# Kernel optimization log

Hardware: AMD Instinct MI355X
Metric: run time of the kernel (lower is better)

Reference implementation:

```python
import jax, jax.numpy as jnp
import numpy as np

EMA_DECAY = 0.99
LOSS_SCALE = 10.0
COMMIT_COEF = 0.25
EPS = 1e-5


def setup_inputs() -> dict:
    key = jax.random.key(0)
    k1, k2, k3 = jax.random.split(key, 3)
    B, S, D, K = 8, 2048, 256, 4096
    z = jax.random.normal(k1, (B, S, D), dtype=jnp.float32)
    attention_mask = jnp.ones((B, S), dtype=jnp.float32)
    codebook = jax.random.normal(k2, (K, D), dtype=jnp.float32)
    ema_count = jnp.ones((K,), dtype=jnp.float32)
    ema_weight = codebook.copy()  # torch: ema_weight = codebook.weight.data.clone()
    return {"z": z, "attention_mask": attention_mask, "codebook": codebook,
            "ema_count": ema_count, "ema_weight": ema_weight}


def reference(z, attention_mask, codebook, ema_count, ema_weight):
    B, S, D = z.shape
    K = codebook.shape[0]
    flat = z.reshape(-1, D)                       # [N, D], N = B*S
    # squared euclidean distances to codebook: [N, K]
    distances = (jnp.sum(flat * flat, axis=1, keepdims=True)
                 - 2.0 * flat @ codebook.T
                 + jnp.sum(codebook * codebook, axis=1))
    indices = jnp.argmin(distances, axis=1)       # [N] int
    quantized = codebook[indices].reshape(B, S, D)

    # EMA accumulation (training path). Instead of materializing the NxK
    # one-hot and doing encodings.T @ flat, use segment sums (same math).
    mask_flat = attention_mask.reshape(-1)        # [N]
    n = jax.ops.segment_sum(mask_flat, indices, num_segments=K)            # [K]
    dw = jax.ops.segment_sum(flat * mask_flat[:, None], indices,
                             num_segments=K)                               # [K, D]

    new_count = ema_count * EMA_DECAY + (1.0 - EMA_DECAY) * n
    total = jnp.sum(new_count)
    new_count = (new_count + EPS) / (total + K * EPS) * total
    new_weight = ema_weight * EMA_DECAY + (1.0 - EMA_DECAY) * dw

    # commitment loss (quantized detached)
    loss_tok = jnp.mean((z - jax.lax.stop_gradient(quantized)) ** 2, axis=-1)  # [B,S]
    quantize_loss = LOSS_SCALE * COMMIT_COEF * jnp.sum(loss_tok * attention_mask) / jnp.sum(attention_mask)

    # straight-through estimator
    out = z + jax.lax.stop_gradient(quantized - z)
    return out, indices, quantize_loss, new_count, new_weight
```

## Files before the change

kernel.cpp:

```cpp
#include <hip/hip_runtime.h>
#include <hip/hip_fp16.h>
#include <cstdint>
#include <cstddef>


#define N_TOK 16384
#define DIM   256
#define K_CB  4096

typedef _Float16 h8    __attribute__((ext_vector_type(8)));
typedef float    f32x4 __attribute__((ext_vector_type(4)));
typedef float    f32x16 __attribute__((ext_vector_type(16)));

#define WS_ZF      0u
#define WS_CP      8388608u
#define WS_CN      10485760u
#define WS_NRM     10502144u
#define WS_CAND    10633216u
#define WS_COUNT   12730368u
#define WS_SLOTS   12746752u
#define WS_NACC    29523968u
#define WS_NB      29540352u
#define WS_LPART   29540368u
#define WS_MPART   29556752u
#define WS_NBPART  29573136u

__device__ __forceinline__ void gload_lds16(const void* g, void* l) {
  __builtin_amdgcn_global_load_lds(
      (const __attribute__((address_space(1))) uint32_t*)g,
      (__attribute__((address_space(3))) uint32_t*)l, 16, 0, 0);
}

__global__ void vq_split_z(const float* __restrict__ z, unsigned short* __restrict__ zf,
                           float2* __restrict__ nrm) {
  int t = blockIdx.x * 256 + threadIdx.x;
  int tok = t >> 5, c = t & 31;
  const float4* zp = reinterpret_cast<const float4*>(z) + (size_t)tok * 64 + c * 2;
  float4 va = zp[0], vb = zp[1];
  float x[8] = {va.x, va.y, va.z, va.w, vb.x, vb.y, vb.z, vb.w};
  union { _Float16 h[8]; uint4 u; } a;
  float s1 = 0.f, s2 = 0.f;
#pragma unroll
  for (int i = 0; i < 8; ++i) {
    _Float16 h1 = (_Float16)x[i];
    float lo = (x[i] - (float)h1) * 2048.0f;
    a.h[i] = h1;
    s1 += (float)h1 * (float)h1;
    s2 += lo * lo;
  }
  size_t off = (size_t)(tok >> 7) * 65536u + (size_t)(c >> 1) * 4096u
             + (size_t)(tok & 127) * 32u + (size_t)(c & 1) * 16u;
  *reinterpret_cast<uint4*>((unsigned char*)zf + off) = a.u;
#pragma unroll
  for (int o = 1; o < 32; o <<= 1) { s1 += __shfl_xor(s1, o); s2 += __shfl_xor(s2, o); }
  if (c == 0) nrm[tok] = make_float2(sqrtf(s1), sqrtf(s2));
}

__global__ void vq_split_c(const float* __restrict__ cb, unsigned short* __restrict__ cp1,
                           float* __restrict__ cn1, float2* __restrict__ nbpart) {
  __shared__ float sm1[4], sm2[4];
  int w = threadIdx.x >> 6, l = threadIdx.x & 63;
  int row = blockIdx.x * 4 + w;
  float4 v = reinterpret_cast<const float4*>(cb)[row * 64 + l];
  float x[4] = {v.x, v.y, v.z, v.w};
  union { _Float16 h[4]; ushort4 u; } a;
  double ss = 0.0;
  float s1 = 0.f, s2 = 0.f;
#pragma unroll
  for (int i = 0; i < 4; ++i) {
    _Float16 h1 = (_Float16)x[i];
    float lo = (x[i] - (float)h1) * 2048.0f;
    a.h[i] = h1;
    s1 += (float)h1 * (float)h1;
    s2 += lo * lo;
    ss += (double)x[i] * (double)x[i];
  }
  reinterpret_cast<ushort4*>(cp1)[row * 64 + l] = a.u;
  for (int off = 1; off < 64; off <<= 1) {
    s1 += __shfl_xor(s1, off); s2 += __shfl_xor(s2, off); ss += __shfl_xor(ss, off);
  }
  if (l == 0) {
    cn1[row] = (float)ss;
    sm1[w] = s1; sm2[w] = s2;
  }
  __syncthreads();
  if (threadIdx.x == 0) {
    float m1 = fmaxf(fmaxf(sm1[0], sm1[1]), fmaxf(sm1[2], sm1[3]));
    float m2 = fmaxf(fmaxf(sm2[0], sm2[1]), fmaxf(sm2[2], sm2[3]));
    nbpart[blockIdx.x] = make_float2(sqrtf(m1), sqrtf(m2));
  }
}

__global__ void vq_nb_reduce(const float2* __restrict__ nbpart, float* __restrict__ nb) {
  __shared__ float r1[256], r2[256];
  int tid = threadIdx.x;
  float m1 = 0.f, m2 = 0.f;
  for (int i = tid; i < 1024; i += 256) {
    float2 p = nbpart[i];
    m1 = fmaxf(m1, p.x); m2 = fmaxf(m2, p.y);
  }
  r1[tid] = m1; r2[tid] = m2; __syncthreads();
  for (int s = 128; s > 0; s >>= 1) {
    if (tid < s) { r1[tid] = fmaxf(r1[tid], r1[tid + s]); r2[tid] = fmaxf(r2[tid], r2[tid + s]); }
    __syncthreads();
  }
  if (tid == 0) { nb[0] = r1[0]; nb[1] = r2[0]; }
}

__global__ __launch_bounds__(256, 2) void vq_scan(
    const unsigned short* __restrict__ zf, const unsigned short* __restrict__ cp,
    const float* __restrict__ cn1, const float2* __restrict__ nrm,
    float2* __restrict__ cand) {
  __shared__ __align__(1024) unsigned char cbl[2][16384];
  __shared__ __align__(16) float cnl[2][32];

  const int bid  = blockIdx.x;
  const int wgid = (bid & 7) * 256 + (bid >> 3);
  const int tg   = wgid >> 4;
  const int es   = wgid & 15;
  const int tok0 = tg * 128;
  const int e0b  = es * 256;

  const int tx = threadIdx.x;
  const int w = tx >> 6, l = tx & 63;
  const int r = l & 31, h = l >> 5;

  const unsigned char* zg = (const unsigned char*)zf + (size_t)tg * 65536u
                            + (unsigned)(w * 1024 + r * 32 + h * 16);
  h8 zfr[16];
#pragma unroll
  for (int kt = 0; kt < 16; ++kt) {
    const void* p = zg + kt * 4096;
    asm volatile("global_load_dwordx4 %0, %1, off"
                 : "=v"(zfr[kt]) : "v"(p));
  }
  float znr = nrm[tok0 + w * 32 + r].x;
  const float zn = znr * znr;

  const unsigned char* cpb = (const unsigned char*)cp;
  unsigned lo = 0xFFFFFFFFu, hi = 0xFFFFFFFFu;

#define STAGE(T1)                                                           \
  {                                                                         \
    const int e0n = e0b + (T1) * 32;                                        \
    _Pragma("unroll")                                                       \
    for (int j = 0; j < 4; ++j) {                                           \
      int row = (w * 4 + j) * 2 + h;                                        \
      int lc  = r ^ row;                                                    \
      gload_lds16(cpb + (size_t)(e0n + row) * 512 + lc * 16,                \
                  &cbl[(T1) & 1][(w * 4 + j) * 1024]);                      \
    }                                                                       \
    if (tx < 8)                                                             \
      gload_lds16((const unsigned char*)cn1 + (size_t)e0n * 4 + tx * 16,    \
                  &cnl[(T1) & 1][0]);                                       \
  }

#define INIT_ACC(C, BUF)                                                    \
  {                                                                         \
    _Pragma("unroll")                                                       \
    for (int g = 0; g < 4; ++g) {                                           \
      f32x4 cnv = *reinterpret_cast<const f32x4*>(&cnl[(BUF)][g * 8 + 4 * h]); \
      _Pragma("unroll")                                                     \
      for (int q = 0; q < 4; ++q) (C)[g * 4 + q] = -0.5f * (zn + cnv[q]);   \
    }                                                                       \
  }

#define MFMA_TILE(C, BUF)                                                   \
  {                                                                         \
    _Pragma("unroll")                                                       \
    for (int kt = 0; kt < 16; ++kt) {                                       \
      int sc = (kt * 2 + h) ^ r;                                            \
      h8 af = *reinterpret_cast<const h8*>(&cbl[(BUF)][r * 512 + sc * 16]); \
      (C) = __builtin_amdgcn_mfma_f32_32x32x16_f16(af, zfr[kt], (C), 0, 0, 0); \
    }                                                                       \
  }

#define SELECT_PREV(P, TPREV)                                               \
  {                                                                         \
    _Pragma("unroll")                                                       \
    for (int i = 0; i < 16; ++i) {                                          \
      unsigned eloc = (unsigned)((TPREV) * 32 + ((i & 3) + 8 * (i >> 2) + 4 * h)); \
      unsigned key = (__float_as_uint((P)[i]) & 0xFFFFFF00u) | eloc;        \
      unsigned mx = lo > key ? lo : key;                                    \
      lo = lo < key ? lo : key;                                             \
      hi = hi < mx ? hi : mx;                                               \
    }                                                                       \
  }

#define TILE_BODY(T, CUR, PRV, DOSEL)                                       \
  {                                                                         \
    if ((T) < 7) STAGE((T) + 1);                                            \
    INIT_ACC(CUR, (T) & 1);                                                 \
    MFMA_TILE(CUR, (T) & 1);                                                \
    if (DOSEL) SELECT_PREV(PRV, (T) - 1);                                   \
    __syncthreads();                                                        \
  }

  STAGE(0);
  __syncthreads();

  f32x16 accA, accB;
  for (int tt = 0; tt < 4; ++tt) {
    TILE_BODY(2 * tt,     accA, accB, (tt > 0));
    TILE_BODY(2 * tt + 1, accB, accA, true);
  }
  SELECT_PREV(accB, 7);

#undef TILE_BODY
#undef SELECT_PREV
#undef MFMA_TILE
#undef INIT_ACC
#undef STAGE

  {
    unsigned olo = __shfl_xor(lo, 32), ohi = __shfl_xor(hi, 32);
    unsigned mx = lo > olo ? lo : olo;
    lo = lo < olo ? lo : olo;
    hi = hi < ohi ? hi : ohi;
    hi = hi < mx ? hi : mx;
    if (h == 0) {
      int token = tok0 + w * 32 + r;
      cand[(size_t)token * 16 + es] =
          make_float2(__uint_as_float(lo), __uint_as_float(hi));
    }
  }
}

__global__ void vq_merge(
    const float2* __restrict__ cand, const float* __restrict__ z,
    const float* __restrict__ mask, const float* __restrict__ codebook,
    const float2* __restrict__ nrm, const float* __restrict__ nb,
    float* __restrict__ out0, float* __restrict__ out_idx,
    int* __restrict__ count, int* __restrict__ slots,
    float* __restrict__ loss_part, float* __restrict__ mask_part) {
  __shared__ float ls[4], ms[4];
  int w = threadIdx.x >> 6, l = threadIdx.x & 63;
  int token = blockIdx.x * 4 + w;

  float2 rec = cand[(size_t)token * 16 + (l & 15)];
  unsigned k1 = __float_as_uint(rec.x), k2 = __float_as_uint(rec.y);
  float rv1 = -2.0f * __uint_as_float(k1 & 0xFFFFFF00u);
  float rv2 = -2.0f * __uint_as_float(k2 & 0xFFFFFF00u);
  int   ri1 = (l & 15) * 256 + (int)(k1 & 0xFFu);
  int   ri2 = (l & 15) * 256 + (int)(k2 & 0xFFu);
  float m_a = rv1;
  for (int o = 1; o < 16; o <<= 1) m_a = fminf(m_a, __shfl_xor(m_a, o));

  float2 nh = nrm[token];
  float NB1 = nb[0], NB2 = nb[1];
  float E = 2.0f * ((nh.x * NB2 + nh.y * NB1) * (1.0f / 2048.0f)
                    + nh.y * NB2 * (1.0f / 4194304.0f));
  float thr = m_a * 1.0001f + 2.0f * E * 1.05f + 0.1f;

  float4 zv = reinterpret_cast<const float4*>(z)[(size_t)token * 64 + l];

  unsigned long long c1 = __ballot((l < 16) && (rv1 <= thr));
  unsigned long long c2 = __ballot((l < 16) && (rv2 <= thr));
  double bd = 1e300; int bi = 0x7fffffff;
  while (c1 | c2) {
    int k;
    if (c1) { int s = __ffsll(c1) - 1; c1 &= c1 - 1; k = __shfl(ri1, s); }
    else    { int s = __ffsll(c2) - 1; c2 &= c2 - 1; k = __shfl(ri2, s); }
    float4 cv = reinterpret_cast<const float4*>(codebook)[(size_t)k * 64 + l];
    double d0 = (double)zv.x - cv.x, d1 = (double)zv.y - cv.y;
    double d2 = (double)zv.z - cv.z, d3 = (double)zv.w - cv.w;
    double dd = d0 * d0 + d1 * d1 + d2 * d2 + d3 * d3;
    for (int o = 1; o < 64; o <<= 1) dd += __shfl_xor(dd, o);
    if (dd < bd || (dd == bd && k < bi)) { bd = dd; bi = k; }
  }

  float4 cv = reinterpret_cast<const float4*>(codebook)[(size_t)bi * 64 + l];
  reinterpret_cast<float4*>(out0)[(size_t)token * 64 + l] = cv;

  float mk = mask[token];
  if (l == 0) {
    out_idx[token] = (float)bi;
    int pos = atomicAdd(&count[bi], 1);
    if (pos < 1024) slots[(size_t)bi * 1024 + pos] = token;
    ls[w] = mk * (float)bd * (1.0f / 256.0f);
    ms[w] = mk;
  }
  __syncthreads();
  if (threadIdx.x == 0) {
    loss_part[blockIdx.x] = ls[0] + ls[1] + ls[2] + ls[3];
    mask_part[blockIdx.x] = ms[0] + ms[1] + ms[2] + ms[3];
  }
}

__global__ __launch_bounds__(512) void vq_segsum(
    const int* __restrict__ count, const int* __restrict__ slots,
    const float* __restrict__ z, const float* __restrict__ mask,
    const float* __restrict__ ew,
    float* __restrict__ out_weight, float* __restrict__ nacc) {
  __shared__ float4 red[8][64];
  __shared__ float nas[8];
  const int k = blockIdx.x;
  const int w = threadIdx.x >> 6, l = threadIdx.x & 63;
  int e = count[k]; if (e > 1024) e = 1024;
  const int* seg = slots + (size_t)k * 1024;
  const float4* z4 = reinterpret_cast<const float4*>(z);

  float ax = 0.f, ay = 0.f, az = 0.f, aw = 0.f, na = 0.f;
  int i = w;
  for (; i + 8 < e; i += 16) {
    int t0 = seg[i], t1 = seg[i + 8];
    float mk0 = mask[t0], mk1 = mask[t1];
    float4 a4 = z4[(size_t)t0 * 64 + l];
    float4 b4 = z4[(size_t)t1 * 64 + l];
    ax += mk0 * a4.x + mk1 * b4.x;
    ay += mk0 * a4.y + mk1 * b4.y;
    az += mk0 * a4.z + mk1 * b4.z;
    aw += mk0 * a4.w + mk1 * b4.w;
    na += mk0 + mk1;
  }
  if (i < e) {
    int t0 = seg[i];
    float mk0 = mask[t0];
    float4 a4 = z4[(size_t)t0 * 64 + l];
    ax += mk0 * a4.x; ay += mk0 * a4.y; az += mk0 * a4.z; aw += mk0 * a4.w;
    na += mk0;
  }
  red[w][l] = make_float4(ax, ay, az, aw);
  if (l == 0) nas[w] = na;
  __syncthreads();

  if (w == 0) {
    float4 a = red[0][l];
#pragma unroll
    for (int j = 1; j < 8; ++j) {
      float4 b = red[j][l];
      a.x += b.x; a.y += b.y; a.z += b.z; a.w += b.w;
    }
    float4 e4 = reinterpret_cast<const float4*>(ew)[(size_t)k * 64 + l];
    float4 o;
    o.x = 0.99f * e4.x + 0.01f * a.x;
    o.y = 0.99f * e4.y + 0.01f * a.y;
    o.z = 0.99f * e4.z + 0.01f * a.z;
    o.w = 0.99f * e4.w + 0.01f * a.w;
    reinterpret_cast<float4*>(out_weight)[(size_t)k * 64 + l] = o;
    if (l == 0) {
      float nn = 0.f;
#pragma unroll
      for (int j = 0; j < 8; ++j) nn += nas[j];
      nacc[k] = nn;
    }
  }
}

__global__ void vq_finish_count(const float* __restrict__ ec, const float* __restrict__ nacc,
                                const float* __restrict__ loss_part,
                                const float* __restrict__ mask_part,
                                float* __restrict__ out_count, float* __restrict__ out_loss) {
  __shared__ float nc_s[K_CB];
  __shared__ float red[256];
  int tid = threadIdx.x;
  float part = 0.f;
  for (int i = tid; i < K_CB; i += 256) {
    float nc = 0.99f * ec[i] + 0.01f * nacc[i];
    nc_s[i] = nc; part += nc;
  }
  red[tid] = part; __syncthreads();
  for (int s = 128; s > 0; s >>= 1) { if (tid < s) red[tid] += red[tid + s]; __syncthreads(); }
  float total = red[0];
  float scale = total / (total + (float)K_CB * 1e-5f);
  for (int i = tid; i < K_CB; i += 256) out_count[i] = (nc_s[i] + 1e-5f) * scale;
  __syncthreads();

  float ln = 0.f, lm = 0.f;
  for (int i = tid; i < 4096; i += 256) { ln += loss_part[i]; lm += mask_part[i]; }
  red[tid] = ln; __syncthreads();
  for (int s = 128; s > 0; s >>= 1) { if (tid < s) red[tid] += red[tid + s]; __syncthreads(); }
  ln = red[0]; __syncthreads();
  red[tid] = lm; __syncthreads();
  for (int s = 128; s > 0; s >>= 1) { if (tid < s) red[tid] += red[tid + s]; __syncthreads(); }
  lm = red[0];
  if (tid == 0) out_loss[0] = 2.5f * ln / lm;
}

extern "C" void kernel_launch(void* const* d_in, const int* in_sizes, int n_in,
                              void* d_out, int out_size, void* d_ws, size_t ws_size,
                              hipStream_t stream) {
  const float* z          = (const float*)d_in[0];
  const float* mask       = (const float*)d_in[1];
  const float* codebook   = (const float*)d_in[2];
  const float* ema_count  = (const float*)d_in[3];
  const float* ema_weight = (const float*)d_in[4];

  float* out        = (float*)d_out;
  float* out0       = out;
  float* out_idx    = out + 4194304;
  float* out_loss   = out + 4210688;
  float* out_count  = out + 4210689;
  float* out_weight = out + 4214785;

  char* ws = (char*)d_ws;
  unsigned short* zf  = (unsigned short*)(ws + WS_ZF);
  unsigned short* cp1 = (unsigned short*)(ws + WS_CP);
  float*  cn1    = (float*) (ws + WS_CN);
  float2* nrm    = (float2*)(ws + WS_NRM);
  float2* cand   = (float2*)(ws + WS_CAND);
  int*    count  = (int*)   (ws + WS_COUNT);
  int*    slots  = (int*)   (ws + WS_SLOTS);
  float*  nacc   = (float*) (ws + WS_NACC);
  float*  nbmax  = (float*) (ws + WS_NB);
  float*  lpart  = (float*) (ws + WS_LPART);
  float*  mpart  = (float*) (ws + WS_MPART);
  float2* nbpart = (float2*)(ws + WS_NBPART);

  (void)hipMemsetAsync(ws + WS_COUNT, 0, 16384, stream);

  vq_split_z<<<2048, 256, 0, stream>>>(z, zf, nrm);
  vq_split_c<<<1024, 256, 0, stream>>>(codebook, cp1, cn1, nbpart);
  vq_nb_reduce<<<1, 256, 0, stream>>>(nbpart, nbmax);
  vq_scan<<<2048, 256, 0, stream>>>(zf, cp1, cn1, nrm, cand);
  vq_merge<<<4096, 256, 0, stream>>>(cand, z, mask, codebook, nrm, nbmax,
                                     out0, out_idx, count, slots, lpart, mpart);
  vq_segsum<<<4096, 512, 0, stream>>>(count, slots, z, mask, ema_weight,
                                      out_weight, nacc);
  vq_finish_count<<<1, 256, 0, stream>>>(ema_count, nacc, lpart, mpart,
                                         out_count, out_loss);
}
```

Baseline: 105.9 us.

## Retile VQ scan to 256-token x 128-code blocks with whole tile preloaded in LDS

The scan kernel now uses 512-thread blocks covering 256 tokens against 128 codebook entries, instead of 128 tokens against 256 entries. The block's full 64KB codebook slice is loaded into dynamic LDS once, up front, which removes the double-buffered per-tile staging and the per-tile barriers. Candidate records grow from 16 to 32 splits per token, so the merge kernel and workspace offsets change to match. In exchange, LDS use and block size go up, which may lower occupancy, and loads no longer overlap with MFMA work inside a block.

```diff
diff --git a/kernel.cpp b/kernel.cpp
--- a/kernel.cpp
+++ b/kernel.cpp
@@ -17,13 +17,13 @@
 #define WS_CN      10485760u
 #define WS_NRM     10502144u
 #define WS_CAND    10633216u
-#define WS_COUNT   12730368u
-#define WS_SLOTS   12746752u
-#define WS_NACC    29523968u
-#define WS_NB      29540352u
-#define WS_LPART   29540368u
-#define WS_MPART   29556752u
-#define WS_NBPART  29573136u
+#define WS_COUNT   14827520u
+#define WS_SLOTS   14843904u
+#define WS_NACC    31621120u
+#define WS_NB      31637504u
+#define WS_LPART   31637520u
+#define WS_MPART   31653904u
+#define WS_NBPART  31670288u
 
 __device__ __forceinline__ void gload_lds16(const void* g, void* l) {
   __builtin_amdgcn_global_load_lds(
@@ -107,26 +107,28 @@
   if (tid == 0) { nb[0] = r1[0]; nb[1] = r2[0]; }
 }
 
-__global__ __launch_bounds__(256, 2) void vq_scan(
+__global__ __launch_bounds__(512, 2) void vq_scan(
     const unsigned short* __restrict__ zf, const unsigned short* __restrict__ cp,
     const float* __restrict__ cn1, const float2* __restrict__ nrm,
     float2* __restrict__ cand) {
-  __shared__ __align__(1024) unsigned char cbl[2][16384];
-  __shared__ __align__(16) float cnl[2][32];
+  extern __shared__ __align__(1024) unsigned char lds[];
+  unsigned char* cbl = lds;
+  float* cnl = reinterpret_cast<float*>(lds + 65536);
 
   const int bid  = blockIdx.x;
   const int wgid = (bid & 7) * 256 + (bid >> 3);
-  const int tg   = wgid >> 4;
-  const int es   = wgid & 15;
-  const int tok0 = tg * 128;
-  const int e0b  = es * 256;
+  const int tg   = wgid >> 5;
+  const int es   = wgid & 31;
+  const int tok0 = tg * 256;
+  const int e0b  = es * 128;
 
   const int tx = threadIdx.x;
   const int w = tx >> 6, l = tx & 63;
   const int r = l & 31, h = l >> 5;
 
-  const unsigned char* zg = (const unsigned char*)zf + (size_t)tg * 65536u
-                            + (unsigned)(w * 1024 + r * 32 + h * 16);
+  const unsigned char* zg = (const unsigned char*)zf
+      + (size_t)(tg * 2 + (w >> 2)) * 65536u
+      + (unsigned)((((w & 3) * 32 + r) * 32) + h * 16);
   h8 zfr[16];
 #pragma unroll
   for (int kt = 0; kt < 16; ++kt) {
@@ -138,79 +140,42 @@
   const float zn = znr * znr;
 
   const unsigned char* cpb = (const unsigned char*)cp;
+#pragma unroll
+  for (int j = 0; j < 8; ++j) {
+    int row = j * 16 + w * 2 + (l >> 5);
+    int lc  = (l & 31) ^ (row & 31);
+    gload_lds16(cpb + (size_t)(e0b + row) * 512 + lc * 16,
+                &cbl[(j * 16 + w * 2) * 512]);
+  }
+  if (tx < 32)
+    gload_lds16((const unsigned char*)cn1 + (size_t)e0b * 4 + tx * 16, cnl);
+  __syncthreads();
+
   unsigned lo = 0xFFFFFFFFu, hi = 0xFFFFFFFFu;
-
-#define STAGE(T1)                                                           \
-  {                                                                         \
-    const int e0n = e0b + (T1) * 32;                                        \
-    _Pragma("unroll")                                                       \
-    for (int j = 0; j < 4; ++j) {                                           \
-      int row = (w * 4 + j) * 2 + h;                                        \
-      int lc  = r ^ row;                                                    \
-      gload_lds16(cpb + (size_t)(e0n + row) * 512 + lc * 16,                \
-                  &cbl[(T1) & 1][(w * 4 + j) * 1024]);                      \
-    }                                                                       \
-    if (tx < 8)                                                             \
-      gload_lds16((const unsigned char*)cn1 + (size_t)e0n * 4 + tx * 16,    \
-                  &cnl[(T1) & 1][0]);                                       \
-  }
-
-#define INIT_ACC(C, BUF)                                                    \
-  {                                                                         \
-    _Pragma("unroll")                                                       \
-    for (int g = 0; g < 4; ++g) {                                           \
-      f32x4 cnv = *reinterpret_cast<const f32x4*>(&cnl[(BUF)][g * 8 + 4 * h]); \
-      _Pragma("unroll")                                                     \
-      for (int q = 0; q < 4; ++q) (C)[g * 4 + q] = -0.5f * (zn + cnv[q]);   \
-    }                                                                       \
-  }
-
-#define MFMA_TILE(C, BUF)                                                   \
-  {                                                                         \
-    _Pragma("unroll")                                                       \
-    for (int kt = 0; kt < 16; ++kt) {                                       \
-      int sc = (kt * 2 + h) ^ r;                                            \
-      h8 af = *reinterpret_cast<const h8*>(&cbl[(BUF)][r * 512 + sc * 16]); \
-      (C) = __builtin_amdgcn_mfma_f32_32x32x16_f16(af, zfr[kt], (C), 0, 0, 0); \
-    }                                                                       \
-  }
-
-#define SELECT_PREV(P, TPREV)                                               \
-  {                                                                         \
-    _Pragma("unroll")                                                       \
-    for (int i = 0; i < 16; ++i) {                                          \
-      unsigned eloc = (unsigned)((TPREV) * 32 + ((i & 3) + 8 * (i >> 2) + 4 * h)); \
-      unsigned key = (__float_as_uint((P)[i]) & 0xFFFFFF00u) | eloc;        \
-      unsigned mx = lo > key ? lo : key;                                    \
-      lo = lo < key ? lo : key;                                             \
-      hi = hi < mx ? hi : mx;                                               \
-    }                                                                       \
-  }
-
-#define TILE_BODY(T, CUR, PRV, DOSEL)                                       \
-  {                                                                         \
-    if ((T) < 7) STAGE((T) + 1);                                            \
-    INIT_ACC(CUR, (T) & 1);                                                 \
-    MFMA_TILE(CUR, (T) & 1);                                                \
-    if (DOSEL) SELECT_PREV(PRV, (T) - 1);                                   \
-    __syncthreads();                                                        \
-  }
-
-  STAGE(0);
-  __syncthreads();
-
-  f32x16 accA, accB;
-  for (int tt = 0; tt < 4; ++tt) {
-    TILE_BODY(2 * tt,     accA, accB, (tt > 0));
-    TILE_BODY(2 * tt + 1, accB, accA, true);
-  }
-  SELECT_PREV(accB, 7);
-
-#undef TILE_BODY
-#undef SELECT_PREV
-#undef MFMA_TILE
-#undef INIT_ACC
-#undef STAGE
+#pragma unroll
+  for (int t = 0; t < 4; ++t) {
+    f32x16 acc;
+#pragma unroll
+    for (int g = 0; g < 4; ++g) {
+      f32x4 cnv = *reinterpret_cast<const f32x4*>(&cnl[t * 32 + g * 8 + 4 * h]);
+#pragma unroll
+      for (int q = 0; q < 4; ++q) acc[g * 4 + q] = -0.5f * (zn + cnv[q]);
+    }
+#pragma unroll
+    for (int kt = 0; kt < 16; ++kt) {
+      int sc = (kt * 2 + h) ^ r;
+      h8 af = *reinterpret_cast<const h8*>(&cbl[t * 16384 + r * 512 + sc * 16]);
+      acc = __builtin_amdgcn_mfma_f32_32x32x16_f16(af, zfr[kt], acc, 0, 0, 0);
+    }
+#pragma unroll
+    for (int i = 0; i < 16; ++i) {
+      unsigned eloc = (unsigned)(t * 32 + ((i & 3) + 8 * (i >> 2) + 4 * h));
+      unsigned key = (__float_as_uint(acc[i]) & 0xFFFFFF00u) | eloc;
+      unsigned mx = lo > key ? lo : key;
+      lo = lo < key ? lo : key;
+      hi = hi < mx ? hi : mx;
+    }
+  }
 
   {
     unsigned olo = __shfl_xor(lo, 32), ohi = __shfl_xor(hi, 32);
@@ -220,7 +185,7 @@
     hi = hi < mx ? hi : mx;
     if (h == 0) {
       int token = tok0 + w * 32 + r;
-      cand[(size_t)token * 16 + es] =
+      cand[(size_t)token * 32 + es] =
           make_float2(__uint_as_float(lo), __uint_as_float(hi));
     }
   }
@@ -237,14 +202,14 @@
   int w = threadIdx.x >> 6, l = threadIdx.x & 63;
   int token = blockIdx.x * 4 + w;
 
-  float2 rec = cand[(size_t)token * 16 + (l & 15)];
+  float2 rec = cand[(size_t)token * 32 + (l & 31)];
   unsigned k1 = __float_as_uint(rec.x), k2 = __float_as_uint(rec.y);
   float rv1 = -2.0f * __uint_as_float(k1 & 0xFFFFFF00u);
   float rv2 = -2.0f * __uint_as_float(k2 & 0xFFFFFF00u);
-  int   ri1 = (l & 15) * 256 + (int)(k1 & 0xFFu);
-  int   ri2 = (l & 15) * 256 + (int)(k2 & 0xFFu);
+  int   ri1 = (l & 31) * 128 + (int)(k1 & 0xFFu);
+  int   ri2 = (l & 31) * 128 + (int)(k2 & 0xFFu);
   float m_a = rv1;
-  for (int o = 1; o < 16; o <<= 1) m_a = fminf(m_a, __shfl_xor(m_a, o));
+  for (int o = 1; o < 32; o <<= 1) m_a = fminf(m_a, __shfl_xor(m_a, o));
 
   float2 nh = nrm[token];
   float NB1 = nb[0], NB2 = nb[1];
@@ -254,8 +219,8 @@
 
   float4 zv = reinterpret_cast<const float4*>(z)[(size_t)token * 64 + l];
 
-  unsigned long long c1 = __ballot((l < 16) && (rv1 <= thr));
-  unsigned long long c2 = __ballot((l < 16) && (rv2 <= thr));
+  unsigned long long c1 = __ballot((l < 32) && (rv1 <= thr));
+  unsigned long long c2 = __ballot((l < 32) && (rv2 <= thr));
   double bd = 1e300; int bi = 0x7fffffff;
   while (c1 | c2) {
     int k;
@@ -407,12 +372,14 @@
   float*  mpart  = (float*) (ws + WS_MPART);
   float2* nbpart = (float2*)(ws + WS_NBPART);
 
+  (void)hipFuncSetAttribute((const void*)vq_scan,
+                            hipFuncAttributeMaxDynamicSharedMemorySize, 66048);
   (void)hipMemsetAsync(ws + WS_COUNT, 0, 16384, stream);
 
   vq_split_z<<<2048, 256, 0, stream>>>(z, zf, nrm);
   vq_split_c<<<1024, 256, 0, stream>>>(codebook, cp1, cn1, nbpart);
   vq_nb_reduce<<<1, 256, 0, stream>>>(nbpart, nbmax);
-  vq_scan<<<2048, 256, 0, stream>>>(zf, cp1, cn1, nrm, cand);
+  vq_scan<<<2048, 512, 66048, stream>>>(zf, cp1, cn1, nrm, cand);
   vq_merge<<<4096, 256, 0, stream>>>(cand, z, mask, codebook, nrm, nbmax,
                                      out0, out_idx, count, slots, lpart, mpart);
   vq_segsum<<<4096, 512, 0, stream>>>(count, slots, z, mask, ema_weight,
```

New measurement: 105.5 us. Within noise of the previous version (-0.4%).
